# Optimization experiments

Hardware: AMD Instinct MI355X
Metric: run time of the kernel (lower is better)

## Reference

```python
import jax, jax.numpy as jnp
import numpy as np

QMIN, QMAX = -128, 127  # int8 range, n_bit = 8


def setup_inputs() -> dict:
    key = jax.random.key(0)
    k1, k2, k3, k4 = jax.random.split(key, 4)
    B, S, IN, OUT = 4, 2048, 4096, 4096
    x = jax.random.normal(k1, (B, S, IN), dtype=jnp.float32)
    weight = jax.random.randint(k2, (OUT, IN), QMIN, QMAX + 1, dtype=jnp.int32).astype(jnp.int8)
    scales = (jax.random.uniform(k3, (OUT,), dtype=jnp.float32) * 0.02 + 1e-3)
    zeros = jax.random.randint(k4, (OUT,), -10, 11, dtype=jnp.int32).astype(jnp.float32)
    return {"x": x, "weight": weight, "scales": scales, "zeros": zeros}


def _per_token_dynamic_quant(x):
    # torchao per_token_dynamic_quant: asymmetric int8 quantize per token
    # (over last dim), then dequantize back to float.
    mn = jnp.minimum(jnp.min(x, axis=-1, keepdims=True), 0.0)
    mx = jnp.maximum(jnp.max(x, axis=-1, keepdims=True), 0.0)
    eps = jnp.finfo(jnp.float32).eps
    scale = jnp.maximum((mx - mn) / (QMAX - QMIN), eps)
    zp = jnp.clip(QMIN - jnp.round(mn / scale), QMIN, QMAX)
    q = jnp.clip(jnp.round(x / scale) + zp, QMIN, QMAX)
    return (q - zp) * scale


def reference(x, weight, scales, zeros):
    x_dq = _per_token_dynamic_quant(x.astype(jnp.float32))
    # per-channel (axis 0 = out_features) weight dequant:
    # w_dq[o, i] = (w_int8[o, i] - zeros[o]) * scales[o]
    w_dq = (weight.astype(jnp.float32) - zeros[:, None]) * scales[:, None]
    # F.linear: x @ w_dq.T -> [B, S, OUT]
    return jnp.einsum('bsi,oi->bso', x_dq, w_dq)
```

## Files before the change

### kernel.cpp

```cpp
#include <hip/hip_runtime.h>
#include <stdint.h>

typedef int   v4i __attribute__((ext_vector_type(4)));
typedef float v4f __attribute__((ext_vector_type(4)));

#define TOK_M 8192
#define DIM_K 4096
#define DIM_N 4096

#define GL(src, dst)                                                                   \
  __builtin_amdgcn_global_load_lds((const __attribute__((address_space(1))) void*)(src), \
                                   (__attribute__((address_space(3))) void*)(dst), 16, 0, 0)

__global__ __launch_bounds__(256) void k_pack_w(const int* __restrict__ w,
                                                int8_t* __restrict__ wq,
                                                float* __restrict__ wsumf) {
    __shared__ int sred[4];
    const int row = blockIdx.x;
    const int tid = threadIdx.x;
    const int4* src = (const int4*)(w + (size_t)row * DIM_K);
    unsigned* dst = (unsigned*)(wq + (size_t)row * DIM_K);
    int sum = 0;
#pragma unroll
    for (int c = 0; c < 4; ++c) {
        int4 iv = src[c * 256 + tid];
        sum += iv.x + iv.y + iv.z + iv.w;
        unsigned p = (unsigned)(iv.x & 255) | ((unsigned)(iv.y & 255) << 8) |
                     ((unsigned)(iv.z & 255) << 16) | ((unsigned)(iv.w & 255) << 24);
        dst[c * 256 + tid] = p;
    }
#pragma unroll
    for (int off = 32; off; off >>= 1) sum += __shfl_xor(sum, off);
    if ((tid & 63) == 0) sred[tid >> 6] = sum;
    __syncthreads();
    if (tid == 0) wsumf[row] = (float)(sred[0] + sred[1] + sred[2] + sred[3]);
}

__global__ __launch_bounds__(256) void k_quant(const float* __restrict__ x,
                                               int8_t* __restrict__ q,
                                               float* __restrict__ sA,
                                               float* __restrict__ sB,
                                               float* __restrict__ sC) {
    __shared__ float redf[8];
    __shared__ int   redi[4];
    __shared__ float bcast[2];
    const int tok = blockIdx.x;
    const int tid = threadIdx.x;
    const v4f* xr = (const v4f*)(x + (size_t)tok * DIM_K);
    v4f v[4];
    float mn = 0.0f, mx = 0.0f;
#pragma unroll
    for (int c = 0; c < 4; ++c) {
        v[c] = xr[c * 256 + tid];
#pragma unroll
        for (int j = 0; j < 4; ++j) {
            mn = fminf(mn, v[c][j]);
            mx = fmaxf(mx, v[c][j]);
        }
    }
#pragma unroll
    for (int off = 32; off; off >>= 1) {
        mn = fminf(mn, __shfl_xor(mn, off));
        mx = fmaxf(mx, __shfl_xor(mx, off));
    }
    const int wid = tid >> 6;
    if ((tid & 63) == 0) { redf[wid] = mn; redf[4 + wid] = mx; }
    __syncthreads();
    if (tid == 0) {
        float m0 = fminf(fminf(redf[0], redf[1]), fminf(redf[2], redf[3]));
        float m1 = fmaxf(fmaxf(redf[4], redf[5]), fmaxf(redf[6], redf[7]));
        float scale = fmaxf((m1 - m0) / 255.0f, 1.1920928955078125e-07f);
        float zpf = -128.0f - rintf(m0 / scale);
        zpf = fminf(fmaxf(zpf, -128.0f), 127.0f);
        bcast[0] = scale; bcast[1] = zpf;
    }
    __syncthreads();
    const float scale = bcast[0];
    const float zpf   = bcast[1];
    const float inv   = 1.0f / scale;
    int qs = 0;
    unsigned* qo = (unsigned*)(q + (size_t)tok * DIM_K);
#pragma unroll
    for (int c = 0; c < 4; ++c) {
        unsigned p = 0;
#pragma unroll
        for (int j = 0; j < 4; ++j) {
            float qf = rintf(v[c][j] * inv) + zpf;
            qf = fminf(fmaxf(qf, -128.0f), 127.0f);
            int qi = (int)qf;
            qs += qi;
            p |= ((unsigned)(qi & 255)) << (8 * j);
        }
        qo[c * 256 + tid] = p;
    }
#pragma unroll
    for (int off = 32; off; off >>= 1) qs += __shfl_xor(qs, off);
    if ((tid & 63) == 0) redi[wid] = qs;
    __syncthreads();
    if (tid == 0) {
        int qtot = redi[0] + redi[1] + redi[2] + redi[3];
        sA[tok] = scale;
        sB[tok] = scale * zpf;
        sC[tok] = scale * ((float)qtot - 4096.0f * zpf);
    }
}

#define MM4(AF, M)                                                                  \
    acc[M][0] = __builtin_amdgcn_mfma_i32_16x16x64_i8(AF, bf0, acc[M][0], 0, 0, 0); \
    acc[M][1] = __builtin_amdgcn_mfma_i32_16x16x64_i8(AF, bf1, acc[M][1], 0, 0, 0); \
    acc[M][2] = __builtin_amdgcn_mfma_i32_16x16x64_i8(AF, bf2, acc[M][2], 0, 0, 0); \
    acc[M][3] = __builtin_amdgcn_mfma_i32_16x16x64_i8(AF, bf3, acc[M][3], 0, 0, 0);

__global__ __launch_bounds__(512, 2) void k_gemm(const int8_t* __restrict__ A,
                                                 const int8_t* __restrict__ B,
                                                 const float* __restrict__ sA,
                                                 const float* __restrict__ sB,
                                                 const float* __restrict__ sC,
                                                 const float* __restrict__ wsumf,
                                                 const float* __restrict__ scales,
                                                 const float* __restrict__ zeros,
                                                 float* __restrict__ out) {
    extern __shared__ int8_t lds[];
    const int tid = threadIdx.x;
    const int l = tid & 63;
    const int wid = tid >> 6;

    const int xcd = blockIdx.x & 7;
    const int idx = blockIdx.x >> 3;
    const int tm = ((xcd >> 1) * 8 + (idx & 7)) * 256;
    const int tn = ((xcd & 1) * 8 + (idx >> 3)) * 256;

    const int sr  = tid >> 2;
    const int scg = (tid & 3) ^ ((tid >> 3) & 3);
    const int8_t* aS0 = A + (size_t)(tm + sr) * DIM_K + scg * 16;
    const int8_t* aS1 = A + (size_t)(tm + 128 + sr) * DIM_K + scg * 16;
    const int8_t* bS0 = B + (size_t)(tn + sr) * DIM_K + scg * 16;
    const int8_t* bS1 = B + (size_t)(tn + 128 + sr) * DIM_K + scg * 16;
    const int dA0 = tid * 16;
    const int dA1 = 8192 + tid * 16;

    const int i  = l & 15;
    const int ch = l >> 4;
    const int pos = ch ^ ((i >> 1) & 3);
    const int wm = (wid >> 2) * 128;
    const int wn = (wid & 3) * 64;
    const int aOff = (wm + i) * 64 + pos * 16;
    const int bOff = 16384 + (wn + i) * 64 + pos * 16;

    v4i acc[8][4] = {};

    GL(aS0, lds + dA0);          GL(aS1, lds + dA1);
    GL(bS0, lds + 16384 + dA0);  GL(bS1, lds + 16384 + dA1);
    GL(aS0 + 64, lds + 32768 + dA0);          GL(aS1 + 64, lds + 32768 + dA1);
    GL(bS0 + 64, lds + 32768 + 16384 + dA0);  GL(bS1 + 64, lds + 32768 + 16384 + dA1);
    asm volatile("s_waitcnt vmcnt(4)" ::: "memory");
    __builtin_amdgcn_s_barrier();

    int cb = 0, sb = 2;
    for (int kt = 0; kt < 64; ++kt) {
        const int koff = kt * 64 + 128;
        int8_t* Sc = lds + cb * 32768;
        int8_t* St = lds + sb * 32768;
        const bool doStage = (kt < 62);
        v4i af0, af1, af2, af3, bf0, bf1, bf2, bf3;

        if (doStage) { GL(aS0 + koff, St + dA0); GL(aS1 + koff, St + dA1); }
        bf0 = *(const v4i*)(Sc + bOff);
        bf1 = *(const v4i*)(Sc + bOff + 1024);
        bf2 = *(const v4i*)(Sc + bOff + 2048);
        bf3 = *(const v4i*)(Sc + bOff + 3072);
        af0 = *(const v4i*)(Sc + aOff);
        af1 = *(const v4i*)(Sc + aOff + 1024);
        af2 = *(const v4i*)(Sc + aOff + 2048);
        af3 = *(const v4i*)(Sc + aOff + 3072);
        __builtin_amdgcn_sched_barrier(0);
        __builtin_amdgcn_s_barrier();
        __builtin_amdgcn_s_setprio(1);
        MM4(af0, 0) MM4(af1, 1) MM4(af2, 2) MM4(af3, 3)
        __builtin_amdgcn_s_setprio(0);
        __builtin_amdgcn_sched_barrier(0);
        __builtin_amdgcn_s_barrier();

        if (doStage) { GL(bS0 + koff, St + 16384 + dA0); GL(bS1 + koff, St + 16384 + dA1); }
        af0 = *(const v4i*)(Sc + aOff + 4096);
        af1 = *(const v4i*)(Sc + aOff + 5120);
        af2 = *(const v4i*)(Sc + aOff + 6144);
        af3 = *(const v4i*)(Sc + aOff + 7168);
        __builtin_amdgcn_sched_barrier(0);
        __builtin_amdgcn_s_barrier();
        __builtin_amdgcn_s_setprio(1);
        MM4(af0, 4) MM4(af1, 5) MM4(af2, 6) MM4(af3, 7)
        __builtin_amdgcn_s_setprio(0);
        __builtin_amdgcn_sched_barrier(0);
        if (kt < 62) { asm volatile("s_waitcnt vmcnt(4)" ::: "memory"); }
        else         { asm volatile("s_waitcnt vmcnt(0)" ::: "memory"); }
        __builtin_amdgcn_s_barrier();

        cb = (cb == 2) ? 0 : cb + 1;
        sb = (sb == 2) ? 0 : sb + 1;
    }

    const int gr0 = tm + wm + ch * 4;
    const int gc0 = tn + wn + i;
    float scl[4], zr[4], wsm[4];
#pragma unroll
    for (int n = 0; n < 4; ++n) {
        const int gc = gc0 + n * 16;
        scl[n] = scales[gc]; zr[n] = zeros[gc]; wsm[n] = wsumf[gc];
    }
#pragma unroll
    for (int m = 0; m < 8; ++m) {
#pragma unroll
        for (int j = 0; j < 4; ++j) {
            const int gr = gr0 + m * 16 + j;
            const float ra = sA[gr], rb = sB[gr], rc = sC[gr];
            float* orow = out + (size_t)gr * DIM_N;
#pragma unroll
            for (int n = 0; n < 4; ++n)
                orow[gc0 + n * 16] =
                    scl[n] * (ra * (float)acc[m][n][j] - rb * wsm[n] - rc * zr[n]);
        }
    }
}

extern "C" void kernel_launch(void* const* d_in, const int* in_sizes, int n_in,
                              void* d_out, int out_size, void* d_ws, size_t ws_size,
                              hipStream_t stream) {
    const float* x      = (const float*)d_in[0];
    const int*   w      = (const int*)d_in[1];
    const float* scales = (const float*)d_in[2];
    const float* zeros  = (const float*)d_in[3];
    float* out = (float*)d_out;

    uint8_t* ws = (uint8_t*)d_ws;
    int8_t* q  = (int8_t*)ws;
    int8_t* wq = (int8_t*)(ws + (size_t)TOK_M * DIM_K);
    float* fbuf = (float*)(ws + (size_t)TOK_M * DIM_K + (size_t)DIM_N * DIM_K);
    float* sA    = fbuf;
    float* sB    = fbuf + TOK_M;
    float* sC    = fbuf + 2 * TOK_M;
    float* wsumf = fbuf + 3 * TOK_M;

    k_pack_w<<<DIM_N, 256, 0, stream>>>(w, wq, wsumf);
    k_quant<<<TOK_M, 256, 0, stream>>>(x, q, sA, sB, sC);
    k_gemm<<<512, 512, 98304, stream>>>(q, wq, sA, sB, sC, wsumf, scales, zeros, out);
}
```

Before: 407.4 us.

## Switch int8 GEMM to 32x32x32 MFMA and drop intra-iteration barriers

Replaces the 16x16x64 int8 MFMA tiling with 32x32x32 MFMA instructions, giving each wave a 4x2 grid of 32x32 accumulators, and rewrites the LDS fragment addressing and epilogue row mapping to match. All four global-to-LDS stage loads are now issued at the start of each k-iteration. The mid-iteration barriers, sched_barriers and setprio hints are removed, leaving one barrier per iteration. The goal is fewer LDS fragment reads per MFMA and less synchronisation. The trade-off is that the compiler now schedules freely without explicit interleaving, which may change how well MFMA work overlaps with the loads.

```diff
diff --git a/kernel.cpp b/kernel.cpp
--- a/kernel.cpp
+++ b/kernel.cpp
@@ -1,8 +1,9 @@
 #include <hip/hip_runtime.h>
 #include <stdint.h>
 
-typedef int   v4i __attribute__((ext_vector_type(4)));
-typedef float v4f __attribute__((ext_vector_type(4)));
+typedef int   v4i  __attribute__((ext_vector_type(4)));
+typedef int   v16i __attribute__((ext_vector_type(16)));
+typedef float v4f  __attribute__((ext_vector_type(4)));
 
 #define TOK_M 8192
 #define DIM_K 4096
@@ -105,12 +106,6 @@
     }
 }
 
-#define MM4(AF, M)                                                                  \
-    acc[M][0] = __builtin_amdgcn_mfma_i32_16x16x64_i8(AF, bf0, acc[M][0], 0, 0, 0); \
-    acc[M][1] = __builtin_amdgcn_mfma_i32_16x16x64_i8(AF, bf1, acc[M][1], 0, 0, 0); \
-    acc[M][2] = __builtin_amdgcn_mfma_i32_16x16x64_i8(AF, bf2, acc[M][2], 0, 0, 0); \
-    acc[M][3] = __builtin_amdgcn_mfma_i32_16x16x64_i8(AF, bf3, acc[M][3], 0, 0, 0);
-
 __global__ __launch_bounds__(512, 2) void k_gemm(const int8_t* __restrict__ A,
                                                  const int8_t* __restrict__ B,
                                                  const float* __restrict__ sA,
@@ -139,15 +134,17 @@
     const int dA0 = tid * 16;
     const int dA1 = 8192 + tid * 16;
 
-    const int i  = l & 15;
-    const int ch = l >> 4;
-    const int pos = ch ^ ((i >> 1) & 3);
+    const int r32 = l & 31;
+    const int kh  = l >> 5;
+    const int f   = (r32 >> 1) & 3;
+    const int p0  = (0 + kh) ^ f;
+    const int p1  = (2 + kh) ^ f;
     const int wm = (wid >> 2) * 128;
     const int wn = (wid & 3) * 64;
-    const int aOff = (wm + i) * 64 + pos * 16;
-    const int bOff = 16384 + (wn + i) * 64 + pos * 16;
-
-    v4i acc[8][4] = {};
+    const int aBase = (wm + r32) * 64;
+    const int bBase = 16384 + (wn + r32) * 64;
+
+    v16i acc[4][2] = {};
 
     GL(aS0, lds + dA0);          GL(aS1, lds + dA1);
     GL(bS0, lds + 16384 + dA0);  GL(bS1, lds + 16384 + dA1);
@@ -159,39 +156,46 @@
     int cb = 0, sb = 2;
     for (int kt = 0; kt < 64; ++kt) {
         const int koff = kt * 64 + 128;
-        int8_t* Sc = lds + cb * 32768;
+        const int8_t* Sc = lds + cb * 32768;
         int8_t* St = lds + sb * 32768;
-        const bool doStage = (kt < 62);
-        v4i af0, af1, af2, af3, bf0, bf1, bf2, bf3;
-
-        if (doStage) { GL(aS0 + koff, St + dA0); GL(aS1 + koff, St + dA1); }
-        bf0 = *(const v4i*)(Sc + bOff);
-        bf1 = *(const v4i*)(Sc + bOff + 1024);
-        bf2 = *(const v4i*)(Sc + bOff + 2048);
-        bf3 = *(const v4i*)(Sc + bOff + 3072);
-        af0 = *(const v4i*)(Sc + aOff);
-        af1 = *(const v4i*)(Sc + aOff + 1024);
-        af2 = *(const v4i*)(Sc + aOff + 2048);
-        af3 = *(const v4i*)(Sc + aOff + 3072);
-        __builtin_amdgcn_sched_barrier(0);
-        __builtin_amdgcn_s_barrier();
-        __builtin_amdgcn_s_setprio(1);
-        MM4(af0, 0) MM4(af1, 1) MM4(af2, 2) MM4(af3, 3)
-        __builtin_amdgcn_s_setprio(0);
-        __builtin_amdgcn_sched_barrier(0);
-        __builtin_amdgcn_s_barrier();
-
-        if (doStage) { GL(bS0 + koff, St + 16384 + dA0); GL(bS1 + koff, St + 16384 + dA1); }
-        af0 = *(const v4i*)(Sc + aOff + 4096);
-        af1 = *(const v4i*)(Sc + aOff + 5120);
-        af2 = *(const v4i*)(Sc + aOff + 6144);
-        af3 = *(const v4i*)(Sc + aOff + 7168);
-        __builtin_amdgcn_sched_barrier(0);
-        __builtin_amdgcn_s_barrier();
-        __builtin_amdgcn_s_setprio(1);
-        MM4(af0, 4) MM4(af1, 5) MM4(af2, 6) MM4(af3, 7)
-        __builtin_amdgcn_s_setprio(0);
-        __builtin_amdgcn_sched_barrier(0);
+
+        if (kt < 62) {
+            GL(aS0 + koff, St + dA0);
+            GL(aS1 + koff, St + dA1);
+            GL(bS0 + koff, St + 16384 + dA0);
+            GL(bS1 + koff, St + 16384 + dA1);
+        }
+
+        v4i a0k0 = *(const v4i*)(Sc + aBase +    0 + p0 * 16);
+        v4i a1k0 = *(const v4i*)(Sc + aBase + 2048 + p0 * 16);
+        v4i a2k0 = *(const v4i*)(Sc + aBase + 4096 + p0 * 16);
+        v4i a3k0 = *(const v4i*)(Sc + aBase + 6144 + p0 * 16);
+        v4i b0k0 = *(const v4i*)(Sc + bBase +    0 + p0 * 16);
+        v4i b1k0 = *(const v4i*)(Sc + bBase + 2048 + p0 * 16);
+        v4i a0k1 = *(const v4i*)(Sc + aBase +    0 + p1 * 16);
+        v4i a1k1 = *(const v4i*)(Sc + aBase + 2048 + p1 * 16);
+        v4i a2k1 = *(const v4i*)(Sc + aBase + 4096 + p1 * 16);
+        v4i a3k1 = *(const v4i*)(Sc + aBase + 6144 + p1 * 16);
+        v4i b0k1 = *(const v4i*)(Sc + bBase +    0 + p1 * 16);
+        v4i b1k1 = *(const v4i*)(Sc + bBase + 2048 + p1 * 16);
+
+        acc[0][0] = __builtin_amdgcn_mfma_i32_32x32x32_i8(a0k0, b0k0, acc[0][0], 0, 0, 0);
+        acc[0][1] = __builtin_amdgcn_mfma_i32_32x32x32_i8(a0k0, b1k0, acc[0][1], 0, 0, 0);
+        acc[1][0] = __builtin_amdgcn_mfma_i32_32x32x32_i8(a1k0, b0k0, acc[1][0], 0, 0, 0);
+        acc[1][1] = __builtin_amdgcn_mfma_i32_32x32x32_i8(a1k0, b1k0, acc[1][1], 0, 0, 0);
+        acc[2][0] = __builtin_amdgcn_mfma_i32_32x32x32_i8(a2k0, b0k0, acc[2][0], 0, 0, 0);
+        acc[2][1] = __builtin_amdgcn_mfma_i32_32x32x32_i8(a2k0, b1k0, acc[2][1], 0, 0, 0);
+        acc[3][0] = __builtin_amdgcn_mfma_i32_32x32x32_i8(a3k0, b0k0, acc[3][0], 0, 0, 0);
+        acc[3][1] = __builtin_amdgcn_mfma_i32_32x32x32_i8(a3k0, b1k0, acc[3][1], 0, 0, 0);
+        acc[0][0] = __builtin_amdgcn_mfma_i32_32x32x32_i8(a0k1, b0k1, acc[0][0], 0, 0, 0);
+        acc[0][1] = __builtin_amdgcn_mfma_i32_32x32x32_i8(a0k1, b1k1, acc[0][1], 0, 0, 0);
+        acc[1][0] = __builtin_amdgcn_mfma_i32_32x32x32_i8(a1k1, b0k1, acc[1][0], 0, 0, 0);
+        acc[1][1] = __builtin_amdgcn_mfma_i32_32x32x32_i8(a1k1, b1k1, acc[1][1], 0, 0, 0);
+        acc[2][0] = __builtin_amdgcn_mfma_i32_32x32x32_i8(a2k1, b0k1, acc[2][0], 0, 0, 0);
+        acc[2][1] = __builtin_amdgcn_mfma_i32_32x32x32_i8(a2k1, b1k1, acc[2][1], 0, 0, 0);
+        acc[3][0] = __builtin_amdgcn_mfma_i32_32x32x32_i8(a3k1, b0k1, acc[3][0], 0, 0, 0);
+        acc[3][1] = __builtin_amdgcn_mfma_i32_32x32x32_i8(a3k1, b1k1, acc[3][1], 0, 0, 0);
+
         if (kt < 62) { asm volatile("s_waitcnt vmcnt(4)" ::: "memory"); }
         else         { asm volatile("s_waitcnt vmcnt(0)" ::: "memory"); }
         __builtin_amdgcn_s_barrier();
@@ -200,25 +204,24 @@
         sb = (sb == 2) ? 0 : sb + 1;
     }
 
-    const int gr0 = tm + wm + ch * 4;
-    const int gc0 = tn + wn + i;
-    float scl[4], zr[4], wsm[4];
-#pragma unroll
-    for (int n = 0; n < 4; ++n) {
-        const int gc = gc0 + n * 16;
+    const int gc0 = tn + wn + r32;
+    float scl[2], zr[2], wsm[2];
+#pragma unroll
+    for (int n = 0; n < 2; ++n) {
+        const int gc = gc0 + n * 32;
         scl[n] = scales[gc]; zr[n] = zeros[gc]; wsm[n] = wsumf[gc];
     }
 #pragma unroll
-    for (int m = 0; m < 8; ++m) {
-#pragma unroll
-        for (int j = 0; j < 4; ++j) {
-            const int gr = gr0 + m * 16 + j;
+    for (int m = 0; m < 4; ++m) {
+#pragma unroll
+        for (int reg = 0; reg < 16; ++reg) {
+            const int gr = tm + wm + m * 32 + (reg & 3) + 8 * (reg >> 2) + 4 * kh;
             const float ra = sA[gr], rb = sB[gr], rc = sC[gr];
             float* orow = out + (size_t)gr * DIM_N;
 #pragma unroll
-            for (int n = 0; n < 4; ++n)
-                orow[gc0 + n * 16] =
-                    scl[n] * (ra * (float)acc[m][n][j] - rb * wsm[n] - rc * zr[n]);
+            for (int n = 0; n < 2; ++n)
+                orow[gc0 + n * 32] =
+                    scl[n] * (ra * (float)acc[m][n][reg] - rb * wsm[n] - rc * zr[n]);
         }
     }
 }
```

Result: no change. 410.7 us (+0.8%).

## Use 4 waves with 128x128 warp tiles and a single-phase K loop in GEMM

Applied to the files above, without the earlier changes.

The int8 GEMM moves from 8 waves, each computing 128x64, to 4 waves, each computing 128x128 with 64 accumulators. The split two-phase loop with extra barriers and setprio is replaced by one phase that issues all eight async staging loads, reads 8 A and 8 B fragments, and runs 64 MFMAs. This raises per-wave operand reuse and removes intra-iteration barriers. In exchange it uses far more VGPRs (256 accumulator registers), runs one block of 4 waves per CU, and drops explicit scheduling hints, which may reduce latency hiding.

```diff
diff --git a/kernel.cpp b/kernel.cpp
--- a/kernel.cpp
+++ b/kernel.cpp
@@ -105,13 +105,7 @@
     }
 }
 
-#define MM4(AF, M)                                                                  \
-    acc[M][0] = __builtin_amdgcn_mfma_i32_16x16x64_i8(AF, bf0, acc[M][0], 0, 0, 0); \
-    acc[M][1] = __builtin_amdgcn_mfma_i32_16x16x64_i8(AF, bf1, acc[M][1], 0, 0, 0); \
-    acc[M][2] = __builtin_amdgcn_mfma_i32_16x16x64_i8(AF, bf2, acc[M][2], 0, 0, 0); \
-    acc[M][3] = __builtin_amdgcn_mfma_i32_16x16x64_i8(AF, bf3, acc[M][3], 0, 0, 0);
-
-__global__ __launch_bounds__(512, 2) void k_gemm(const int8_t* __restrict__ A,
+__global__ __launch_bounds__(256, 1) void k_gemm(const int8_t* __restrict__ A,
                                                  const int8_t* __restrict__ B,
                                                  const float* __restrict__ sA,
                                                  const float* __restrict__ sB,
@@ -130,69 +124,58 @@
     const int tm = ((xcd >> 1) * 8 + (idx & 7)) * 256;
     const int tn = ((xcd & 1) * 8 + (idx >> 3)) * 256;
 
-    const int sr  = tid >> 2;
-    const int scg = (tid & 3) ^ ((tid >> 3) & 3);
-    const int8_t* aS0 = A + (size_t)(tm + sr) * DIM_K + scg * 16;
-    const int8_t* aS1 = A + (size_t)(tm + 128 + sr) * DIM_K + scg * 16;
-    const int8_t* bS0 = B + (size_t)(tn + sr) * DIM_K + scg * 16;
-    const int8_t* bS1 = B + (size_t)(tn + 128 + sr) * DIM_K + scg * 16;
-    const int dA0 = tid * 16;
-    const int dA1 = 8192 + tid * 16;
+    const int srow = tid >> 2;
+    const int scg  = (tid & 3) ^ ((tid >> 3) & 3);
+    const int8_t* gsrc[8];
+#pragma unroll
+    for (int r = 0; r < 4; ++r)
+        gsrc[r] = A + (size_t)(tm + r * 64 + srow) * DIM_K + scg * 16;
+#pragma unroll
+    for (int r = 0; r < 4; ++r)
+        gsrc[4 + r] = B + (size_t)(tn + r * 64 + srow) * DIM_K + scg * 16;
+    const int dOff = tid * 16;
 
     const int i  = l & 15;
     const int ch = l >> 4;
-    const int pos = ch ^ ((i >> 1) & 3);
-    const int wm = (wid >> 2) * 128;
-    const int wn = (wid & 3) * 64;
-    const int aOff = (wm + i) * 64 + pos * 16;
-    const int bOff = 16384 + (wn + i) * 64 + pos * 16;
-
-    v4i acc[8][4] = {};
-
-    GL(aS0, lds + dA0);          GL(aS1, lds + dA1);
-    GL(bS0, lds + 16384 + dA0);  GL(bS1, lds + 16384 + dA1);
-    GL(aS0 + 64, lds + 32768 + dA0);          GL(aS1 + 64, lds + 32768 + dA1);
-    GL(bS0 + 64, lds + 32768 + 16384 + dA0);  GL(bS1 + 64, lds + 32768 + 16384 + dA1);
-    asm volatile("s_waitcnt vmcnt(4)" ::: "memory");
+    const int pos = (ch ^ ((i >> 1) & 3)) * 16;
+    const int wm = (wid >> 1) * 128;
+    const int wn = (wid & 1) * 128;
+    const int aOff = (wm + i) * 64 + pos;
+    const int bOff = 16384 + (wn + i) * 64 + pos;
+
+    v4i acc[8][8] = {};
+
+#pragma unroll
+    for (int r = 0; r < 8; ++r) GL(gsrc[r], lds + r * 4096 + dOff);
+#pragma unroll
+    for (int r = 0; r < 8; ++r) GL(gsrc[r] + 64, lds + 32768 + r * 4096 + dOff);
+    asm volatile("s_waitcnt vmcnt(8)" ::: "memory");
     __builtin_amdgcn_s_barrier();
 
     int cb = 0, sb = 2;
     for (int kt = 0; kt < 64; ++kt) {
         const int koff = kt * 64 + 128;
-        int8_t* Sc = lds + cb * 32768;
+        const int8_t* Sc = lds + cb * 32768;
         int8_t* St = lds + sb * 32768;
-        const bool doStage = (kt < 62);
-        v4i af0, af1, af2, af3, bf0, bf1, bf2, bf3;
-
-        if (doStage) { GL(aS0 + koff, St + dA0); GL(aS1 + koff, St + dA1); }
-        bf0 = *(const v4i*)(Sc + bOff);
-        bf1 = *(const v4i*)(Sc + bOff + 1024);
-        bf2 = *(const v4i*)(Sc + bOff + 2048);
-        bf3 = *(const v4i*)(Sc + bOff + 3072);
-        af0 = *(const v4i*)(Sc + aOff);
-        af1 = *(const v4i*)(Sc + aOff + 1024);
-        af2 = *(const v4i*)(Sc + aOff + 2048);
-        af3 = *(const v4i*)(Sc + aOff + 3072);
-        __builtin_amdgcn_sched_barrier(0);
-        __builtin_amdgcn_s_barrier();
-        __builtin_amdgcn_s_setprio(1);
-        MM4(af0, 0) MM4(af1, 1) MM4(af2, 2) MM4(af3, 3)
-        __builtin_amdgcn_s_setprio(0);
-        __builtin_amdgcn_sched_barrier(0);
-        __builtin_amdgcn_s_barrier();
-
-        if (doStage) { GL(bS0 + koff, St + 16384 + dA0); GL(bS1 + koff, St + 16384 + dA1); }
-        af0 = *(const v4i*)(Sc + aOff + 4096);
-        af1 = *(const v4i*)(Sc + aOff + 5120);
-        af2 = *(const v4i*)(Sc + aOff + 6144);
-        af3 = *(const v4i*)(Sc + aOff + 7168);
-        __builtin_amdgcn_sched_barrier(0);
-        __builtin_amdgcn_s_barrier();
-        __builtin_amdgcn_s_setprio(1);
-        MM4(af0, 4) MM4(af1, 5) MM4(af2, 6) MM4(af3, 7)
-        __builtin_amdgcn_s_setprio(0);
-        __builtin_amdgcn_sched_barrier(0);
-        if (kt < 62) { asm volatile("s_waitcnt vmcnt(4)" ::: "memory"); }
+
+        if (kt < 62) {
+#pragma unroll
+            for (int r = 0; r < 8; ++r) GL(gsrc[r] + koff, St + r * 4096 + dOff);
+        }
+
+        v4i af[8], bf[8];
+#pragma unroll
+        for (int mi = 0; mi < 8; ++mi) af[mi] = *(const v4i*)(Sc + aOff + mi * 1024);
+#pragma unroll
+        for (int ni = 0; ni < 8; ++ni) bf[ni] = *(const v4i*)(Sc + bOff + ni * 1024);
+#pragma unroll
+        for (int mi = 0; mi < 8; ++mi)
+#pragma unroll
+            for (int ni = 0; ni < 8; ++ni)
+                acc[mi][ni] = __builtin_amdgcn_mfma_i32_16x16x64_i8(
+                    af[mi], bf[ni], acc[mi][ni], 0, 0, 0);
+
+        if (kt < 62) { asm volatile("s_waitcnt vmcnt(8)" ::: "memory"); }
         else         { asm volatile("s_waitcnt vmcnt(0)" ::: "memory"); }
         __builtin_amdgcn_s_barrier();
 
@@ -200,11 +183,10 @@
         sb = (sb == 2) ? 0 : sb + 1;
     }
 
-    const int gr0 = tm + wm + ch * 4;
     const int gc0 = tn + wn + i;
-    float scl[4], zr[4], wsm[4];
-#pragma unroll
-    for (int n = 0; n < 4; ++n) {
+    float scl[8], zr[8], wsm[8];
+#pragma unroll
+    for (int n = 0; n < 8; ++n) {
         const int gc = gc0 + n * 16;
         scl[n] = scales[gc]; zr[n] = zeros[gc]; wsm[n] = wsumf[gc];
     }
@@ -212,11 +194,11 @@
     for (int m = 0; m < 8; ++m) {
 #pragma unroll
         for (int j = 0; j < 4; ++j) {
-            const int gr = gr0 + m * 16 + j;
+            const int gr = tm + wm + m * 16 + ch * 4 + j;
             const float ra = sA[gr], rb = sB[gr], rc = sC[gr];
             float* orow = out + (size_t)gr * DIM_N;
 #pragma unroll
-            for (int n = 0; n < 4; ++n)
+            for (int n = 0; n < 8; ++n)
                 orow[gc0 + n * 16] =
                     scl[n] * (ra * (float)acc[m][n][j] - rb * wsm[n] - rc * zr[n]);
         }
@@ -243,5 +225,5 @@
 
     k_pack_w<<<DIM_N, 256, 0, stream>>>(w, wq, wsumf);
     k_quant<<<TOK_M, 256, 0, stream>>>(x, q, sA, sB, sC);
-    k_gemm<<<512, 512, 98304, stream>>>(q, wq, sA, sB, sC, wsumf, scales, zeros, out);
-}
+    k_gemm<<<512, 256, 98304, stream>>>(q, wq, sA, sB, sC, wsumf, scales, zeros, out);
+}
```

Measured after the change: 509.0 us. 1.25x slower.
